# Optimization experiments

Hardware: AMD Instinct MI355X
Metric: run time of the kernel (lower is better)

Reference implementation:

```python
import jax, jax.numpy as jnp
import numpy as np

EPS_KERNEL = 1e-6
EPS_Z = 1e-6


def softmax_kernel(data, projection_matrix):
    # data: [b,h,l,d], projection_matrix: [m,d]
    data_normalizer = data.shape[-1] ** (-0.25)
    data = data * data_normalizer
    projection = jnp.einsum('bhld,md->bhlm', data, projection_matrix)
    data_squared_norm = jnp.sum(data ** 2, axis=-1, keepdims=True) / 2
    return jnp.exp(projection - data_squared_norm + EPS_KERNEL)


def setup_inputs() -> dict:
    key = jax.random.key(0)
    k1, k2, k3, k4 = jax.random.split(key, 4)
    b, h, l, d, m = 4, 8, 8192, 64, 256
    return {
        'q': jax.random.normal(k1, (b, h, l, d), dtype=jnp.float32),
        'k': jax.random.normal(k2, (b, h, l, d), dtype=jnp.float32),
        'v': jax.random.normal(k3, (b, h, l, d), dtype=jnp.float32),
        'projection_matrix': jax.random.normal(k4, (m, d), dtype=jnp.float32),
    }


def reference(q, k, v, projection_matrix):
    q_prime = softmax_kernel(q, projection_matrix)  # [b,h,l,m]
    k_prime = softmax_kernel(k, projection_matrix)  # [b,h,l,m]
    kv = jnp.einsum('bhlm,bhld->bhmd', k_prime, v)  # [b,h,m,d]
    k_sum = jnp.sum(k_prime, axis=2)                # [b,h,m]
    z_raw = jnp.einsum('bhlm,bhm->bhl', q_prime, k_sum)
    z = 1.0 / (z_raw + EPS_Z)                       # [b,h,l]
    # (q_prime @ kv) scaled per-token by z
    out = jnp.einsum('bhlm,bhmd->bhld', q_prime, kv) * z[..., None]
    return out
```

## Files before the change

### kernel.cpp

```cpp
#include <hip/hip_runtime.h>
#include <hip/hip_bf16.h>


#define BH 32
#define LL 8192
#define DD 64
#define MM 256
#define NRM 0.35355339059327373f
#define SQS 0.0625f
#define EPSK 1e-6f
#define EPSZ 1e-6f

typedef __attribute__((ext_vector_type(8))) short bf16x8;
typedef __attribute__((ext_vector_type(4))) float f32x4;
#define MFMA(a, b, c) __builtin_amdgcn_mfma_f32_16x16x32_bf16(a, b, c, 0, 0, 0)

static __device__ __forceinline__ short f2bf(float x) {
    union { float f; unsigned u; } c{x};
    unsigned r = c.u + 0x7fffu + ((c.u >> 16) & 1u);
    return (short)(r >> 16);
}

static __device__ __forceinline__ void load_pfrags(
    const float* __restrict__ Pm, int wv, int quad, int l16, bf16x8 pb[2][4])
{
#pragma unroll
    for (int ks = 0; ks < 2; ++ks)
#pragma unroll
        for (int mt = 0; mt < 4; ++mt) {
            const float* pr = Pm + (wv * 64 + mt * 16 + l16) * DD + ks * 32 + quad * 8;
            float4 p0 = *(const float4*)pr;
            float4 p1 = *(const float4*)(pr + 4);
            bf16x8 f;
            f[0] = f2bf(p0.x * NRM); f[1] = f2bf(p0.y * NRM);
            f[2] = f2bf(p0.z * NRM); f[3] = f2bf(p0.w * NRM);
            f[4] = f2bf(p1.x * NRM); f[5] = f2bf(p1.y * NRM);
            f[6] = f2bf(p1.z * NRM); f[7] = f2bf(p1.w * NRM);
            pb[ks][mt] = f;
        }
}

__global__ __launch_bounds__(256, 2) void kv_kernel(
    const float* __restrict__ kin, const float* __restrict__ vin,
    const float* __restrict__ Pm, float* __restrict__ kv, float* __restrict__ ksum)
{
    __shared__ short Kb[32 * 72];
    __shared__ short Vt[64 * 40];
    __shared__ short Ktp[256 * 40];
    __shared__ float cl_lds[32];

    const int t = threadIdx.x;
    const int lane = t & 63, wv = t >> 6;
    const int quad = lane >> 4, l16 = lane & 15;
    const int bh = blockIdx.x >> 4, chunk = blockIdx.x & 15;

    bf16x8 pb[2][4];
    load_pfrags(Pm, wv, quad, l16, pb);

    f32x4 kvacc[4][4];
#pragma unroll
    for (int mt = 0; mt < 4; ++mt)
#pragma unroll
        for (int dt = 0; dt < 4; ++dt) kvacc[mt][dt] = (f32x4)0.f;
    float ksacc[4] = {0.f, 0.f, 0.f, 0.f};

    const size_t base = ((size_t)bh * LL + (size_t)chunk * 512) * DD;
    const float* kb = kin + base;
    const float* vb = vin + base;
    const int sl = t >> 4, sd4 = t & 15;

    for (int tile = 0; tile < 16; ++tile) {
        __syncthreads();
#pragma unroll
        for (int half = 0; half < 2; ++half) {
            const int l = sl + half * 16;
            const int gi = (tile * 32 + l) * DD + sd4 * 4;
            float4 kf = *(const float4*)(kb + gi);
            float sq = kf.x * kf.x + kf.y * kf.y + kf.z * kf.z + kf.w * kf.w;
            sq += __shfl_xor(sq, 1); sq += __shfl_xor(sq, 2);
            sq += __shfl_xor(sq, 4); sq += __shfl_xor(sq, 8);
            if (sd4 == 0) cl_lds[l] = EPSK - SQS * sq;
            union { short s[4]; unsigned long long u; } uk;
            uk.s[0] = f2bf(kf.x); uk.s[1] = f2bf(kf.y);
            uk.s[2] = f2bf(kf.z); uk.s[3] = f2bf(kf.w);
            *(unsigned long long*)&Kb[l * 72 + sd4 * 4] = uk.u;
            float4 vf = *(const float4*)(vb + gi);
            Vt[(sd4 * 4 + 0) * 40 + l] = f2bf(vf.x);
            Vt[(sd4 * 4 + 1) * 40 + l] = f2bf(vf.y);
            Vt[(sd4 * 4 + 2) * 40 + l] = f2bf(vf.z);
            Vt[(sd4 * 4 + 3) * 40 + l] = f2bf(vf.w);
        }
        __syncthreads();
        f32x4 pt[2][4];
#pragma unroll
        for (int lt = 0; lt < 2; ++lt)
#pragma unroll
            for (int mt = 0; mt < 4; ++mt) pt[lt][mt] = (f32x4)0.f;
#pragma unroll
        for (int ks = 0; ks < 2; ++ks)
#pragma unroll
            for (int lt = 0; lt < 2; ++lt) {
                bf16x8 af = *(bf16x8*)&Kb[(lt * 16 + l16) * 72 + ks * 32 + quad * 8];
#pragma unroll
                for (int mt = 0; mt < 4; ++mt)
                    pt[lt][mt] = MFMA(af, pb[ks][mt], pt[lt][mt]);
            }
        float cl[2][4];
#pragma unroll
        for (int lt = 0; lt < 2; ++lt)
#pragma unroll
            for (int r = 0; r < 4; ++r) cl[lt][r] = cl_lds[lt * 16 + quad * 4 + r];
#pragma unroll
        for (int lt = 0; lt < 2; ++lt)
#pragma unroll
            for (int mt = 0; mt < 4; ++mt) {
                union { short s[4]; unsigned long long u; } uo;
#pragma unroll
                for (int r = 0; r < 4; ++r) {
                    float w = __expf(pt[lt][mt][r] + cl[lt][r]);
                    ksacc[mt] += w;
                    uo.s[r] = f2bf(w);
                }
                *(unsigned long long*)&Ktp[(wv * 64 + mt * 16 + l16) * 40 + lt * 16 + quad * 4] = uo.u;
            }
        bf16x8 aK[4], bV[4];
#pragma unroll
        for (int mt = 0; mt < 4; ++mt)
            aK[mt] = *(bf16x8*)&Ktp[(wv * 64 + mt * 16 + l16) * 40 + quad * 8];
#pragma unroll
        for (int dt = 0; dt < 4; ++dt)
            bV[dt] = *(bf16x8*)&Vt[(dt * 16 + l16) * 40 + quad * 8];
#pragma unroll
        for (int mt = 0; mt < 4; ++mt)
#pragma unroll
            for (int dt = 0; dt < 4; ++dt)
                kvacc[mt][dt] = MFMA(aK[mt], bV[dt], kvacc[mt][dt]);
    }
    float* kvg = kv + (size_t)bh * MM * DD;
#pragma unroll
    for (int mt = 0; mt < 4; ++mt) {
        float r = ksacc[mt];
        r += __shfl_xor(r, 16); r += __shfl_xor(r, 32);
        if (quad == 0) atomicAdd(ksum + bh * MM + wv * 64 + mt * 16 + l16, r);
#pragma unroll
        for (int dt = 0; dt < 4; ++dt)
#pragma unroll
            for (int rg = 0; rg < 4; ++rg)
                atomicAdd(kvg + (wv * 64 + mt * 16 + quad * 4 + rg) * DD + dt * 16 + l16,
                          kvacc[mt][dt][rg]);
    }
}

__global__ __launch_bounds__(256, 2) void out_kernel(
    const float* __restrict__ qin, const float* __restrict__ Pm,
    const float* __restrict__ kv, const float* __restrict__ ksum,
    float* __restrict__ out)
{
    __shared__ short Qb[32 * 72];
    __shared__ short Qp[32 * 264];
    __shared__ short kvT[64 * 264];
    __shared__ float ks_lds[MM];
    __shared__ float cl_lds[32];
    __shared__ float z_lds[32];

    const int t = threadIdx.x;
    const int lane = t & 63, wv = t >> 6;
    const int quad = lane >> 4, l16 = lane & 15;
    const int bh = blockIdx.x >> 4, chunk = blockIdx.x & 15;

    bf16x8 pb[2][4];
    load_pfrags(Pm, wv, quad, l16, pb);

    const float* kvg = kv + (size_t)bh * MM * DD;
#pragma unroll
    for (int it = 0; it < 16; ++it) {
        int i = t + it * 256;
        int m = i >> 4, d4 = i & 15;
        float4 f = *(const float4*)(kvg + m * DD + d4 * 4);
        kvT[(d4 * 4 + 0) * 264 + m] = f2bf(f.x);
        kvT[(d4 * 4 + 1) * 264 + m] = f2bf(f.y);
        kvT[(d4 * 4 + 2) * 264 + m] = f2bf(f.z);
        kvT[(d4 * 4 + 3) * 264 + m] = f2bf(f.w);
    }
    ks_lds[t] = ksum[bh * MM + t];
    __syncthreads();
    float ksv[4];
#pragma unroll
    for (int mt = 0; mt < 4; ++mt) ksv[mt] = ks_lds[wv * 64 + mt * 16 + l16];

    const size_t base = ((size_t)bh * LL + (size_t)chunk * 512) * DD;
    const float* qb = qin + base;
    float* ob = out + base;
    const int sl = t >> 4, sd4 = t & 15;

    for (int tile = 0; tile < 16; ++tile) {
        __syncthreads();
        if (t < 32) z_lds[t] = 0.f;
#pragma unroll
        for (int half = 0; half < 2; ++half) {
            const int l = sl + half * 16;
            const int gi = (tile * 32 + l) * DD + sd4 * 4;
            float4 qf = *(const float4*)(qb + gi);
            float sq = qf.x * qf.x + qf.y * qf.y + qf.z * qf.z + qf.w * qf.w;
            sq += __shfl_xor(sq, 1); sq += __shfl_xor(sq, 2);
            sq += __shfl_xor(sq, 4); sq += __shfl_xor(sq, 8);
            if (sd4 == 0) cl_lds[l] = EPSK - SQS * sq;
            union { short s[4]; unsigned long long u; } uq;
            uq.s[0] = f2bf(qf.x); uq.s[1] = f2bf(qf.y);
            uq.s[2] = f2bf(qf.z); uq.s[3] = f2bf(qf.w);
            *(unsigned long long*)&Qb[l * 72 + sd4 * 4] = uq.u;
        }
        __syncthreads();
        f32x4 pt[2][4];
#pragma unroll
        for (int lt = 0; lt < 2; ++lt)
#pragma unroll
            for (int mt = 0; mt < 4; ++mt) pt[lt][mt] = (f32x4)0.f;
#pragma unroll
        for (int ks = 0; ks < 2; ++ks)
#pragma unroll
            for (int lt = 0; lt < 2; ++lt) {
                bf16x8 af = *(bf16x8*)&Qb[(lt * 16 + l16) * 72 + ks * 32 + quad * 8];
#pragma unroll
                for (int mt = 0; mt < 4; ++mt)
                    pt[lt][mt] = MFMA(af, pb[ks][mt], pt[lt][mt]);
            }
        float cl[2][4];
#pragma unroll
        for (int lt = 0; lt < 2; ++lt)
#pragma unroll
            for (int r = 0; r < 4; ++r) cl[lt][r] = cl_lds[lt * 16 + quad * 4 + r];
        float zp[2][4] = {{0.f,0.f,0.f,0.f},{0.f,0.f,0.f,0.f}};
#pragma unroll
        for (int lt = 0; lt < 2; ++lt)
#pragma unroll
            for (int mt = 0; mt < 4; ++mt)
#pragma unroll
                for (int r = 0; r < 4; ++r) {
                    float w = __expf(pt[lt][mt][r] + cl[lt][r]);
                    zp[lt][r] += w * ksv[mt];
                    Qp[(lt * 16 + quad * 4 + r) * 264 + wv * 64 + mt * 16 + l16] = f2bf(w);
                }
#pragma unroll
        for (int lt = 0; lt < 2; ++lt)
#pragma unroll
            for (int r = 0; r < 4; ++r) {
                float vz = zp[lt][r];
                vz += __shfl_xor(vz, 1); vz += __shfl_xor(vz, 2);
                vz += __shfl_xor(vz, 4); vz += __shfl_xor(vz, 8);
                if (l16 == 0) atomicAdd(&z_lds[lt * 16 + quad * 4 + r], vz);
            }
        __syncthreads();
        f32x4 oc[2];
        oc[0] = (f32x4)0.f; oc[1] = (f32x4)0.f;
#pragma unroll
        for (int ks = 0; ks < 8; ++ks) {
            bf16x8 bk = *(bf16x8*)&kvT[(wv * 16 + l16) * 264 + ks * 32 + quad * 8];
#pragma unroll
            for (int lt = 0; lt < 2; ++lt) {
                bf16x8 aq = *(bf16x8*)&Qp[(lt * 16 + l16) * 264 + ks * 32 + quad * 8];
                oc[lt] = MFMA(aq, bk, oc[lt]);
            }
        }
#pragma unroll
        for (int lt = 0; lt < 2; ++lt)
#pragma unroll
            for (int r = 0; r < 4; ++r) {
                const int row = lt * 16 + quad * 4 + r;
                const float z = 1.f / (z_lds[row] + EPSZ);
                ob[(size_t)(tile * 32 + row) * DD + wv * 16 + l16] = oc[lt][r] * z;
            }
    }
}

extern "C" void kernel_launch(void* const* d_in, const int* in_sizes, int n_in,
                              void* d_out, int out_size, void* d_ws, size_t ws_size,
                              hipStream_t stream) {
    const float* q  = (const float*)d_in[0];
    const float* k  = (const float*)d_in[1];
    const float* v  = (const float*)d_in[2];
    const float* Pm = (const float*)d_in[3];

    float* kvw = (float*)d_ws;
    float* ksw = kvw + (size_t)BH * MM * DD;

    hipMemsetAsync(d_ws, 0, ((size_t)BH * MM * DD + (size_t)BH * MM) * sizeof(float), stream);
    hipLaunchKernelGGL(kv_kernel, dim3(512), dim3(256), 0, stream, k, v, Pm, kvw, ksw);
    hipLaunchKernelGGL(out_kernel, dim3(512), dim3(256), 0, stream, q, Pm, kvw, ksw, (float*)d_out);
}
```

Measured before the change: 323.9 us.

## Load K/Q MFMA fragments directly from global and double block count

Each wave now loads its K/Q rows straight from global memory into bf16 MFMA A-fragments. The row norm is computed with lane shuffles, which removes the Kb/Qb and cl_lds shared-memory staging and one barrier per tile. The grid doubles to 1024 blocks with 256-row chunks, and launch bounds move to 3 blocks per CU to raise occupancy. The shared-memory atomic z reduction becomes per-wave partial sums added at the end. The trade-offs are redundant global loads across waves (each wave reads the same 32 rows), more global atomics from the smaller chunks, and more register pressure.

```diff
diff --git a/kernel.cpp b/kernel.cpp
--- a/kernel.cpp
+++ b/kernel.cpp
@@ -10,6 +10,10 @@
 #define SQS 0.0625f
 #define EPSK 1e-6f
 #define EPSZ 1e-6f
+
+#define NCHUNK 32
+#define CROWS (LL / NCHUNK)
+#define NTILE (CROWS / 32)
 
 typedef __attribute__((ext_vector_type(8))) short bf16x8;
 typedef __attribute__((ext_vector_type(4))) float f32x4;
@@ -40,19 +44,46 @@
         }
 }
 
-__global__ __launch_bounds__(256, 2) void kv_kernel(
+static __device__ __forceinline__ void load_afrags(
+    const float* __restrict__ xb, int row0, int quad, int l16,
+    bf16x8 af[2][2], float cuse[2][4])
+{
+#pragma unroll
+    for (int lt = 0; lt < 2; ++lt) {
+        const float* pr = xb + (size_t)(row0 + lt * 16 + l16) * DD + quad * 8;
+        float4 f0 = *(const float4*)pr;
+        float4 f1 = *(const float4*)(pr + 4);
+        float4 f2 = *(const float4*)(pr + 32);
+        float4 f3 = *(const float4*)(pr + 36);
+        float sq = f0.x*f0.x + f0.y*f0.y + f0.z*f0.z + f0.w*f0.w
+                 + f1.x*f1.x + f1.y*f1.y + f1.z*f1.z + f1.w*f1.w
+                 + f2.x*f2.x + f2.y*f2.y + f2.z*f2.z + f2.w*f2.w
+                 + f3.x*f3.x + f3.y*f3.y + f3.z*f3.z + f3.w*f3.w;
+        sq += __shfl_xor(sq, 16);
+        sq += __shfl_xor(sq, 32);
+        const float cl = EPSK - SQS * sq;
+#pragma unroll
+        for (int r = 0; r < 4; ++r) cuse[lt][r] = __shfl(cl, quad * 4 + r);
+        bf16x8 a0, a1;
+        a0[0]=f2bf(f0.x); a0[1]=f2bf(f0.y); a0[2]=f2bf(f0.z); a0[3]=f2bf(f0.w);
+        a0[4]=f2bf(f1.x); a0[5]=f2bf(f1.y); a0[6]=f2bf(f1.z); a0[7]=f2bf(f1.w);
+        a1[0]=f2bf(f2.x); a1[1]=f2bf(f2.y); a1[2]=f2bf(f2.z); a1[3]=f2bf(f2.w);
+        a1[4]=f2bf(f3.x); a1[5]=f2bf(f3.y); a1[6]=f2bf(f3.z); a1[7]=f2bf(f3.w);
+        af[lt][0] = a0; af[lt][1] = a1;
+    }
+}
+
+__global__ __launch_bounds__(256, 3) void kv_kernel(
     const float* __restrict__ kin, const float* __restrict__ vin,
     const float* __restrict__ Pm, float* __restrict__ kv, float* __restrict__ ksum)
 {
-    __shared__ short Kb[32 * 72];
     __shared__ short Vt[64 * 40];
     __shared__ short Ktp[256 * 40];
-    __shared__ float cl_lds[32];
 
     const int t = threadIdx.x;
     const int lane = t & 63, wv = t >> 6;
     const int quad = lane >> 4, l16 = lane & 15;
-    const int bh = blockIdx.x >> 4, chunk = blockIdx.x & 15;
+    const int bh = blockIdx.x >> 5, chunk = blockIdx.x & 31;
 
     bf16x8 pb[2][4];
     load_pfrags(Pm, wv, quad, l16, pb);
@@ -64,33 +95,26 @@
         for (int dt = 0; dt < 4; ++dt) kvacc[mt][dt] = (f32x4)0.f;
     float ksacc[4] = {0.f, 0.f, 0.f, 0.f};
 
-    const size_t base = ((size_t)bh * LL + (size_t)chunk * 512) * DD;
+    const size_t base = ((size_t)bh * LL + (size_t)chunk * CROWS) * DD;
     const float* kb = kin + base;
     const float* vb = vin + base;
-    const int sl = t >> 4, sd4 = t & 15;
-
-    for (int tile = 0; tile < 16; ++tile) {
-        __syncthreads();
-#pragma unroll
-        for (int half = 0; half < 2; ++half) {
-            const int l = sl + half * 16;
-            const int gi = (tile * 32 + l) * DD + sd4 * 4;
-            float4 kf = *(const float4*)(kb + gi);
-            float sq = kf.x * kf.x + kf.y * kf.y + kf.z * kf.z + kf.w * kf.w;
-            sq += __shfl_xor(sq, 1); sq += __shfl_xor(sq, 2);
-            sq += __shfl_xor(sq, 4); sq += __shfl_xor(sq, 8);
-            if (sd4 == 0) cl_lds[l] = EPSK - SQS * sq;
-            union { short s[4]; unsigned long long u; } uk;
-            uk.s[0] = f2bf(kf.x); uk.s[1] = f2bf(kf.y);
-            uk.s[2] = f2bf(kf.z); uk.s[3] = f2bf(kf.w);
-            *(unsigned long long*)&Kb[l * 72 + sd4 * 4] = uk.u;
-            float4 vf = *(const float4*)(vb + gi);
-            Vt[(sd4 * 4 + 0) * 40 + l] = f2bf(vf.x);
-            Vt[(sd4 * 4 + 1) * 40 + l] = f2bf(vf.y);
-            Vt[(sd4 * 4 + 2) * 40 + l] = f2bf(vf.z);
-            Vt[(sd4 * 4 + 3) * 40 + l] = f2bf(vf.w);
+    const int lp = t >> 4, sd4 = t & 15;
+
+    for (int tile = 0; tile < NTILE; ++tile) {
+        const int gi = (tile * 32 + 2 * lp) * DD + sd4 * 4;
+        float4 vf0 = *(const float4*)(vb + gi);
+        float4 vf1 = *(const float4*)(vb + gi + DD);
+        bf16x8 Ka[2][2]; float cuse[2][4];
+        load_afrags(kb, tile * 32, quad, l16, Ka, cuse);
+
+        __syncthreads();
+#pragma unroll
+        for (int c = 0; c < 4; ++c) {
+            union { short s[2]; unsigned u; } p;
+            p.s[0] = f2bf((&vf0.x)[c]);
+            p.s[1] = f2bf((&vf1.x)[c]);
+            *(unsigned*)&Vt[(sd4 * 4 + c) * 40 + 2 * lp] = p.u;
         }
-        __syncthreads();
         f32x4 pt[2][4];
 #pragma unroll
         for (int lt = 0; lt < 2; ++lt)
@@ -99,17 +123,10 @@
 #pragma unroll
         for (int ks = 0; ks < 2; ++ks)
 #pragma unroll
-            for (int lt = 0; lt < 2; ++lt) {
-                bf16x8 af = *(bf16x8*)&Kb[(lt * 16 + l16) * 72 + ks * 32 + quad * 8];
+            for (int lt = 0; lt < 2; ++lt)
 #pragma unroll
                 for (int mt = 0; mt < 4; ++mt)
-                    pt[lt][mt] = MFMA(af, pb[ks][mt], pt[lt][mt]);
-            }
-        float cl[2][4];
-#pragma unroll
-        for (int lt = 0; lt < 2; ++lt)
-#pragma unroll
-            for (int r = 0; r < 4; ++r) cl[lt][r] = cl_lds[lt * 16 + quad * 4 + r];
+                    pt[lt][mt] = MFMA(Ka[lt][ks], pb[ks][mt], pt[lt][mt]);
 #pragma unroll
         for (int lt = 0; lt < 2; ++lt)
 #pragma unroll
@@ -117,12 +134,13 @@
                 union { short s[4]; unsigned long long u; } uo;
 #pragma unroll
                 for (int r = 0; r < 4; ++r) {
-                    float w = __expf(pt[lt][mt][r] + cl[lt][r]);
+                    float w = __expf(pt[lt][mt][r] + cuse[lt][r]);
                     ksacc[mt] += w;
                     uo.s[r] = f2bf(w);
                 }
                 *(unsigned long long*)&Ktp[(wv * 64 + mt * 16 + l16) * 40 + lt * 16 + quad * 4] = uo.u;
             }
+        __syncthreads();
         bf16x8 aK[4], bV[4];
 #pragma unroll
         for (int mt = 0; mt < 4; ++mt)
@@ -151,22 +169,20 @@
     }
 }
 
-__global__ __launch_bounds__(256, 2) void out_kernel(
+__global__ __launch_bounds__(256, 3) void out_kernel(
     const float* __restrict__ qin, const float* __restrict__ Pm,
     const float* __restrict__ kv, const float* __restrict__ ksum,
     float* __restrict__ out)
 {
-    __shared__ short Qb[32 * 72];
     __shared__ short Qp[32 * 264];
     __shared__ short kvT[64 * 264];
     __shared__ float ks_lds[MM];
-    __shared__ float cl_lds[32];
-    __shared__ float z_lds[32];
+    __shared__ float z_lds[4 * 32];
 
     const int t = threadIdx.x;
     const int lane = t & 63, wv = t >> 6;
     const int quad = lane >> 4, l16 = lane & 15;
-    const int bh = blockIdx.x >> 4, chunk = blockIdx.x & 15;
+    const int bh = blockIdx.x >> 5, chunk = blockIdx.x & 31;
 
     bf16x8 pb[2][4];
     load_pfrags(Pm, wv, quad, l16, pb);
@@ -188,28 +204,14 @@
 #pragma unroll
     for (int mt = 0; mt < 4; ++mt) ksv[mt] = ks_lds[wv * 64 + mt * 16 + l16];
 
-    const size_t base = ((size_t)bh * LL + (size_t)chunk * 512) * DD;
+    const size_t base = ((size_t)bh * LL + (size_t)chunk * CROWS) * DD;
     const float* qb = qin + base;
     float* ob = out + base;
-    const int sl = t >> 4, sd4 = t & 15;
-
-    for (int tile = 0; tile < 16; ++tile) {
-        __syncthreads();
-        if (t < 32) z_lds[t] = 0.f;
-#pragma unroll
-        for (int half = 0; half < 2; ++half) {
-            const int l = sl + half * 16;
-            const int gi = (tile * 32 + l) * DD + sd4 * 4;
-            float4 qf = *(const float4*)(qb + gi);
-            float sq = qf.x * qf.x + qf.y * qf.y + qf.z * qf.z + qf.w * qf.w;
-            sq += __shfl_xor(sq, 1); sq += __shfl_xor(sq, 2);
-            sq += __shfl_xor(sq, 4); sq += __shfl_xor(sq, 8);
-            if (sd4 == 0) cl_lds[l] = EPSK - SQS * sq;
-            union { short s[4]; unsigned long long u; } uq;
-            uq.s[0] = f2bf(qf.x); uq.s[1] = f2bf(qf.y);
-            uq.s[2] = f2bf(qf.z); uq.s[3] = f2bf(qf.w);
-            *(unsigned long long*)&Qb[l * 72 + sd4 * 4] = uq.u;
-        }
+
+    for (int tile = 0; tile < NTILE; ++tile) {
+        bf16x8 Qa[2][2]; float cuse[2][4];
+        load_afrags(qb, tile * 32, quad, l16, Qa, cuse);
+
         __syncthreads();
         f32x4 pt[2][4];
 #pragma unroll
@@ -219,17 +221,10 @@
 #pragma unroll
         for (int ks = 0; ks < 2; ++ks)
 #pragma unroll
-            for (int lt = 0; lt < 2; ++lt) {
-                bf16x8 af = *(bf16x8*)&Qb[(lt * 16 + l16) * 72 + ks * 32 + quad * 8];
+            for (int lt = 0; lt < 2; ++lt)
 #pragma unroll
                 for (int mt = 0; mt < 4; ++mt)
-                    pt[lt][mt] = MFMA(af, pb[ks][mt], pt[lt][mt]);
-            }
-        float cl[2][4];
-#pragma unroll
-        for (int lt = 0; lt < 2; ++lt)
-#pragma unroll
-            for (int r = 0; r < 4; ++r) cl[lt][r] = cl_lds[lt * 16 + quad * 4 + r];
+                    pt[lt][mt] = MFMA(Qa[lt][ks], pb[ks][mt], pt[lt][mt]);
         float zp[2][4] = {{0.f,0.f,0.f,0.f},{0.f,0.f,0.f,0.f}};
 #pragma unroll
         for (int lt = 0; lt < 2; ++lt)
@@ -237,7 +232,7 @@
             for (int mt = 0; mt < 4; ++mt)
 #pragma unroll
                 for (int r = 0; r < 4; ++r) {
-                    float w = __expf(pt[lt][mt][r] + cl[lt][r]);
+                    float w = __expf(pt[lt][mt][r] + cuse[lt][r]);
                     zp[lt][r] += w * ksv[mt];
                     Qp[(lt * 16 + quad * 4 + r) * 264 + wv * 64 + mt * 16 + l16] = f2bf(w);
                 }
@@ -248,7 +243,7 @@
                 float vz = zp[lt][r];
                 vz += __shfl_xor(vz, 1); vz += __shfl_xor(vz, 2);
                 vz += __shfl_xor(vz, 4); vz += __shfl_xor(vz, 8);
-                if (l16 == 0) atomicAdd(&z_lds[lt * 16 + quad * 4 + r], vz);
+                if (l16 == 0) z_lds[wv * 32 + lt * 16 + quad * 4 + r] = vz;
             }
         __syncthreads();
         f32x4 oc[2];
@@ -267,7 +262,9 @@
 #pragma unroll
             for (int r = 0; r < 4; ++r) {
                 const int row = lt * 16 + quad * 4 + r;
-                const float z = 1.f / (z_lds[row] + EPSZ);
+                const float zr = z_lds[row] + z_lds[32 + row]
+                               + z_lds[64 + row] + z_lds[96 + row];
+                const float z = 1.f / (zr + EPSZ);
                 ob[(size_t)(tile * 32 + row) * DD + wv * 16 + l16] = oc[lt][r] * z;
             }
     }
@@ -285,6 +282,6 @@
     float* ksw = kvw + (size_t)BH * MM * DD;
 
     hipMemsetAsync(d_ws, 0, ((size_t)BH * MM * DD + (size_t)BH * MM) * sizeof(float), stream);
-    hipLaunchKernelGGL(kv_kernel, dim3(512), dim3(256), 0, stream, k, v, Pm, kvw, ksw);
-    hipLaunchKernelGGL(out_kernel, dim3(512), dim3(256), 0, stream, q, Pm, kvw, ksw, (float*)d_out);
-}
+    hipLaunchKernelGGL(kv_kernel, dim3(BH * NCHUNK), dim3(256), 0, stream, k, v, Pm, kvw, ksw);
+    hipLaunchKernelGGL(out_kernel, dim3(BH * NCHUNK), dim3(256), 0, stream, q, Pm, kvw, ksw, (float*)d_out);
+}
```

Result: slower. 390.0 us (+20.4%).
